# Optimization experiments

Hardware: AMD Instinct MI355X
Metric: run time of the kernel (lower is better)

## Reference

```python
import jax, jax.numpy as jnp
import numpy as np

N_NODES = 100000
N_EDGES = 600000
IN_F, HID_F, OUT_F = 128, 128, 64


def setup_inputs() -> dict:
    key = jax.random.key(0)
    ks = jax.random.split(key, 12)
    s = 0.05  # small init scale to keep activations bounded
    return {
        "features": jax.random.normal(ks[0], (N_NODES, IN_F), jnp.float32),
        "edge_src": jax.random.randint(ks[1], (N_EDGES,), 0, N_NODES, jnp.int32),
        "edge_dst": jax.random.randint(ks[2], (N_EDGES,), 0, N_NODES, jnp.int32),
        "W1": jax.random.normal(ks[3], (HID_F, 3 * IN_F), jnp.float32) * s,
        "b1": jnp.zeros((HID_F,), jnp.float32),
        "bn_gamma": jnp.ones((HID_F,), jnp.float32),
        "bn_beta": jnp.zeros((HID_F,), jnp.float32),
        "bn_mean": jnp.zeros((HID_F,), jnp.float32),
        "bn_var": jnp.ones((HID_F,), jnp.float32),
        "W3": jax.random.normal(ks[4], (HID_F, 3 * HID_F), jnp.float32) * s,
        "b3": jnp.zeros((HID_F,), jnp.float32),
        "Wm1": jax.random.normal(ks[5], (HID_F, HID_F), jnp.float32) * s,
        "bm1": jnp.zeros((HID_F,), jnp.float32),
        "Wm2": jax.random.normal(ks[6], (OUT_F, HID_F), jnp.float32) * s,
        "bm2": jnp.zeros((OUT_F,), jnp.float32),
    }


def _cheb_conv(x, W, b, src, dst, dinv, n):
    """DGL ChebConv with k=3, lambda_max=2 (re_norm=1).
    L f = f - D^-1/2 A D^-1/2 f  via gather-scatter on the edge list."""
    def lap(f):
        agg = jax.ops.segment_sum((f * dinv)[src], dst, num_segments=n)
        return f - agg * dinv
    X0 = x
    X1 = -lap(X0)                 # X1 = -re_norm*L(X0) + (re_norm-1)*X0, re_norm=1
    X2 = -2.0 * lap(X1) - X0      # X2 = -2*re_norm*L(X1) + 2*(re_norm-1)*X1 - X0
    Xt = jnp.concatenate([X0, X1, X2], axis=1)  # [n, 3*in]
    return Xt @ W.T + b


def reference(features, edge_src, edge_dst, W1, b1, bn_gamma, bn_beta,
              bn_mean, bn_var, W3, b3, Wm1, bm1, Wm2, bm2):
    n = features.shape[0]
    deg = jax.ops.segment_sum(jnp.ones_like(edge_dst, jnp.float32), edge_dst,
                              num_segments=n)
    dinv = jnp.clip(deg, 1.0, None) ** -0.5  # D^{-1/2}, in-degree (DGL)
    dinv = dinv[:, None]

    x = jax.nn.relu(_cheb_conv(features, W1, b1, edge_src, edge_dst, dinv, n))
    # BatchNorm1d (eval mode)
    x = (x - bn_mean) * jax.lax.rsqrt(bn_var + 1e-5) * bn_gamma + bn_beta
    # NOTE: original early-stopping loop never updates x -> dead code, omitted.
    x_res = x
    x = jax.nn.relu(_cheb_conv(x, W3, b3, edge_src, edge_dst, dinv, n))
    x = x + x_res  # dropout is identity in eval mode
    # MLP head
    h = jax.nn.relu(x @ Wm1.T + bm1)
    return h @ Wm2.T + bm2
```

## Files before the change

kernel.cpp:

```cpp
#include <hip/hip_runtime.h>
#include <cstdint>
#include <cstddef>

#define NF 128
#define SCAN_B 256

typedef __attribute__((ext_vector_type(4))) float f32x4;
typedef __attribute__((ext_vector_type(8))) short bf16x8;

#define GL2LDS16(g, l) __builtin_amdgcn_global_load_lds(                     \
    (const __attribute__((address_space(1))) unsigned*)(g),                  \
    (__attribute__((address_space(3))) unsigned*)(l), 16, 0, 0)

static __device__ inline float bf2f(short u) {
    union { unsigned u; float f; } v;
    v.u = ((unsigned)(unsigned short)u) << 16;
    return v.f;
}
static __device__ inline short f2bf(float f) {
    union { float f; unsigned u; } v; v.f = f;
    unsigned r = v.u + 0x7FFF + ((v.u >> 16) & 1);
    return (short)(r >> 16);
}
static __device__ inline float u2f(unsigned u) {
    union { unsigned u; float f; } v; v.u = u; return v.f;
}
static __device__ inline unsigned f2u(float f) {
    union { float f; unsigned u; } v; v.f = f; return v.u;
}
static __device__ inline unsigned packbf(float lo, float hi) {
    unsigned ul = f2u(lo), uh = f2u(hi);
    ul = ul + 0x7FFF + ((ul >> 16) & 1);
    uh = uh + 0x7FFF + ((uh >> 16) & 1);
    return (ul >> 16) | (uh & 0xFFFF0000u);
}


static __global__ __launch_bounds__(256) void k_pro(
    const int* __restrict__ dst, int ne, int* __restrict__ counts,
    const float* __restrict__ feat, short* __restrict__ fbf, int n8, int nbE, int nbF,
    const float* __restrict__ w1, const float* __restrict__ w3,
    const float* __restrict__ wm1, const float* __restrict__ wm2,
    short* __restrict__ o1, short* __restrict__ o3,
    short* __restrict__ om1, short* __restrict__ om2) {
    int b = blockIdx.x;
    if (b < nbE) {
        int e = b * 256 + threadIdx.x;
        if (e < ne) atomicAdd(&counts[dst[e]], 1);
        return;
    }
    b -= nbE;
    if (b < nbF) {
        int i = b * 256 + threadIdx.x;
        if (i < n8) {
            f32x4 a = *(const f32x4*)&feat[(size_t)i * 8];
            f32x4 c = *(const f32x4*)&feat[(size_t)i * 8 + 4];
            bf16x8 r;
            r[0] = f2bf(a[0]); r[1] = f2bf(a[1]); r[2] = f2bf(a[2]); r[3] = f2bf(a[3]);
            r[4] = f2bf(c[0]); r[5] = f2bf(c[1]); r[6] = f2bf(c[2]); r[7] = f2bf(c[3]);
            *(bf16x8*)&fbf[(size_t)i * 8] = r;
        }
        return;
    }
    b -= nbF;
    int i = b * 256 + threadIdx.x;
    if (i < 12288) {
        const float* x = (i < 6144) ? w1 : w3;
        short* y       = (i < 6144) ? o1 : o3;
        int ii = (i < 6144) ? i : i - 6144;
        int r = ii / 48, c = ii % 48;
        int kt = c * 8, seg = kt >> 7, o = kt & 127;
        const float* base = x + (size_t)r * 384;
        float c0, c1, c2;
        if (seg == 0)      { c0 = 1.f;  c1 = -1.f; c2 = 1.f;  }
        else if (seg == 1) { c0 = 0.f;  c1 = 1.f;  c2 = -4.f; }
        else               { c0 = 0.f;  c1 = 0.f;  c2 = 2.f;  }
        bf16x8 rr;
#pragma unroll
        for (int h = 0; h < 2; ++h) {
            f32x4 a0 = *(const f32x4*)&base[o + h * 4];
            f32x4 a1 = *(const f32x4*)&base[128 + o + h * 4];
            f32x4 a2 = *(const f32x4*)&base[256 + o + h * 4];
#pragma unroll
            for (int j = 0; j < 4; ++j)
                rr[h * 4 + j] = f2bf(c0 * a0[j] + c1 * a1[j] + c2 * a2[j]);
        }
        *(bf16x8*)&y[(size_t)r * 384 + kt] = rr;
        return;
    }
    const float* x; short* y; int off;
    if (i < 14336) { x = wm1; y = om1; off = i - 12288; }
    else           { x = wm2; y = om2; off = i - 14336; }
    f32x4 a = *(const f32x4*)&x[(size_t)off * 8];
    f32x4 c = *(const f32x4*)&x[(size_t)off * 8 + 4];
    bf16x8 r;
    r[0] = f2bf(a[0]); r[1] = f2bf(a[1]); r[2] = f2bf(a[2]); r[3] = f2bf(a[3]);
    r[4] = f2bf(c[0]); r[5] = f2bf(c[1]); r[6] = f2bf(c[2]); r[7] = f2bf(c[3]);
    *(bf16x8*)&y[(size_t)off * 8] = r;
}


static __global__ void k_scan1(const int* __restrict__ counts, int n,
                               int* __restrict__ row_off, int* __restrict__ bsum) {
    __shared__ int s[SCAN_B];
    int t = threadIdx.x;
    int base = blockIdx.x * SCAN_B;
    int v = (base + t < n) ? counts[base + t] : 0;
    s[t] = v;
    __syncthreads();
    for (int off = 1; off < SCAN_B; off <<= 1) {
        int x = 0;
        if (t >= off) x = s[t - off];
        __syncthreads();
        if (t >= off) s[t] += x;
        __syncthreads();
    }
    if (base + t < n) row_off[base + t] = s[t] - v;
    if (t == SCAN_B - 1) bsum[blockIdx.x] = s[t];
}

static __global__ void k_scan2(int* __restrict__ bsum, int nb) {
    __shared__ int s[512];
    int t = threadIdx.x;
    int v = (t < nb) ? bsum[t] : 0;
    s[t] = v;
    __syncthreads();
    for (int off = 1; off < 512; off <<= 1) {
        int x = 0;
        if (t >= off) x = s[t - off];
        __syncthreads();
        if (t >= off) s[t] += x;
        __syncthreads();
    }
    if (t < nb) bsum[t] = s[t] - v;
}

static __global__ void k_scan3(int* __restrict__ row_off, const int* __restrict__ bsum,
                               int n, int ne, int* __restrict__ cursor,
                               const int* __restrict__ counts, float* __restrict__ dinv) {
    int i = blockIdx.x * SCAN_B + threadIdx.x;
    if (i < n) {
        int v = row_off[i] + bsum[blockIdx.x];
        row_off[i] = v;
        cursor[i] = v;
        float d = fmaxf((float)counts[i], 1.0f);
        dinv[i] = rsqrtf(d);
    }
    if (i == 0) row_off[n] = ne;
}

static __global__ void k_fill(const int* __restrict__ src, const int* __restrict__ dst, int ne,
                              int* __restrict__ cursor, int2* __restrict__ csrw,
                              const float* __restrict__ dinv) {
    int e = blockIdx.x * blockDim.x + threadIdx.x;
    if (e < ne) {
        int d = dst[e];
        int s = src[e];
        int p = atomicAdd(&cursor[d], 1);
        csrw[p] = make_int2(s, (int)f2u(dinv[s]));
    }
}


static __global__ __launch_bounds__(256) void k_lap(
    const short* __restrict__ Xin,
    const int* __restrict__ row_off, const int2* __restrict__ csrw,
    const float* __restrict__ dinv,
    short* __restrict__ out, int n) {
    int node = blockIdx.x * 4 + (threadIdx.x >> 6);
    if (node >= n) return;
    int l = threadIdx.x & 63;
    const unsigned* Xu = (const unsigned*)Xin;
    int e0 = row_off[node], e1 = row_off[node + 1];
    int deg = e1 - e0;

    int myi = 0; int mydv = 0;
    if (l < deg && l < 64) {
        int2 q = csrw[e0 + l];
        myi = q.x; mydv = q.y;
    }

    float s0 = 0.f, s1 = 0.f;
    int dcap = deg < 64 ? deg : 64;
    for (int base = 0; base < dcap; base += 8) {
        unsigned v[8]; float dv[8];
#pragma unroll
        for (int j = 0; j < 8; ++j) {
            int jj = base + j;
            bool act = (jj < dcap);
            int lane = act ? jj : base;
            int src = __builtin_amdgcn_readlane(myi, lane);
            unsigned dvb = __builtin_amdgcn_readlane(mydv, lane);
            dv[j] = act ? u2f(dvb) : 0.f;
            v[j] = Xu[(size_t)src * 64 + l];
        }
#pragma unroll
        for (int j = 0; j < 8; ++j) {
            s0 += u2f(v[j] << 16) * dv[j];
            s1 += u2f(v[j] & 0xFFFF0000u) * dv[j];
        }
    }
    for (int base = e0 + 64; base < e1; base += 8) {
        int m = e1 - base;
        int2 qq = make_int2(0, 0);
        if (l < 8 && l < m) qq = csrw[base + l];
        unsigned v[8]; float dv[8];
#pragma unroll
        for (int j = 0; j < 8; ++j) {
            int src = __shfl(qq.x, j, 64);
            int dvb = __shfl(qq.y, j, 64);
            bool act = (j < m);
            if (!act) src = 0;
            dv[j] = act ? u2f((unsigned)dvb) : 0.f;
            v[j] = Xu[(size_t)src * 64 + l];
        }
#pragma unroll
        for (int j = 0; j < 8; ++j) {
            s0 += u2f(v[j] << 16) * dv[j];
            s1 += u2f(v[j] & 0xFFFF0000u) * dv[j];
        }
    }

    float di = dinv[node];
    ((unsigned*)out)[(size_t)node * 64 + l] = packbf(s0 * di, s1 * di);
}


static __global__ __launch_bounds__(512) void k_gemm_conv(
    const short* __restrict__ X0, const short* __restrict__ X1, const short* __restrict__ X2,
    const short* __restrict__ Wbf, const float* __restrict__ bias,
    const float* __restrict__ bng, const float* __restrict__ bnb,
    const float* __restrict__ bnm, const float* __restrict__ bnv,
    int M, short* __restrict__ out) {
    __shared__ short As[2][128 * 32];
    __shared__ short Bs[2][128 * 32];

    const int nwg = gridDim.x;
    const int q = nwg >> 3, r = nwg & 7;
    const int xcd = blockIdx.x & 7, slot = blockIdx.x >> 3;
    const int flat = (xcd < r ? xcd * (q + 1) : r * (q + 1) + (xcd - r) * q) + slot;
    const int m0 = flat * 128;

    const int t = threadIdx.x;
    const int wv = t >> 6;
    const int ln = t & 63;
    const int wr = wv >> 2;
    const int wc = wv & 3;
    const int lr = ln & 15;
    const int lk = ln >> 4;

    const short* segs[3] = {X0, X1, X2};

    f32x4 acc[4][2];
#pragma unroll
    for (int i = 0; i < 4; ++i)
#pragma unroll
        for (int j = 0; j < 2; ++j) acc[i][j] = (f32x4){0.f, 0.f, 0.f, 0.f};

    auto issue = [&](int buf, int kt) {
        const short* Xp = segs[kt >> 7];
        const int klocal = kt & 127;
#pragma unroll
        for (int j = 0; j < 2; ++j) {
            int g = wv * 2 + j;
            int c = g * 64 + ln;
            if (g < 8) {
                int row = c >> 2, sl = c & 3;
                int gm = m0 + row;
                if (gm > M - 1) gm = M - 1;
                const short* src = &Xp[(size_t)gm * 128 + klocal + ((sl ^ ((row >> 1) & 3)) * 8)];
                GL2LDS16(src, &As[buf][g * 512]);
            } else {
                int cb = c - 512;
                int row = cb >> 2, sl = cb & 3;
                const short* src = &Wbf[(size_t)row * 384 + kt + ((sl ^ ((row >> 1) & 3)) * 8)];
                GL2LDS16(src, &Bs[buf][(g - 8) * 512]);
            }
        }
    };
    auto compute = [&](int buf) {
        bf16x8 af[4], bfr[2];
#pragma unroll
        for (int fi = 0; fi < 4; ++fi) {
            int row = wr * 64 + fi * 16 + lr;
            af[fi] = *(const bf16x8*)&As[buf][row * 32 + ((lk ^ ((row >> 1) & 3)) * 8)];
        }
#pragma unroll
        for (int fj = 0; fj < 2; ++fj) {
            int row = wc * 32 + fj * 16 + lr;
            bfr[fj] = *(const bf16x8*)&Bs[buf][row * 32 + ((lk ^ ((row >> 1) & 3)) * 8)];
        }
#pragma unroll
        for (int fi = 0; fi < 4; ++fi)
#pragma unroll
            for (int fj = 0; fj < 2; ++fj)
                acc[fi][fj] = __builtin_amdgcn_mfma_f32_16x16x32_bf16(af[fi], bfr[fj], acc[fi][fj], 0, 0, 0);
    };

    issue(0, 0);
    __syncthreads();
#pragma unroll
    for (int tgt = 0; tgt < 12; ++tgt) {
        if (tgt < 11) issue((tgt + 1) & 1, (tgt + 1) * 32);
        compute(tgt & 1);
        __syncthreads();
    }

#pragma unroll
    for (int fi = 0; fi < 4; ++fi) {
#pragma unroll
        for (int reg = 0; reg < 4; ++reg) {
            int gm = m0 + wr * 64 + fi * 16 + lk * 4 + reg;
            if (gm >= M) continue;
#pragma unroll
            for (int fj = 0; fj < 2; ++fj) {
                int gn = wc * 32 + fj * 16 + lr;
                float y = fmaxf(acc[fi][fj][reg] + bias[gn], 0.f);
                float sc = rsqrtf(bnv[gn] + 1e-5f) * bng[gn];
                y = (y - bnm[gn]) * sc + bnb[gn];
                out[(size_t)gm * 128 + gn] = f2bf(y);
            }
        }
    }
}


static __global__ __launch_bounds__(512) void k_gemm_mlp(
    const short* __restrict__ X0, const short* __restrict__ X1, const short* __restrict__ X2,
    const short* __restrict__ Wbf, const float* __restrict__ bias,
    const short* __restrict__ res,
    const short* __restrict__ Wm1bf, const float* __restrict__ bm1,
    const short* __restrict__ Wm2bf, const float* __restrict__ bm2,
    int M, float* __restrict__ out) {
    __shared__ __align__(16) short smem[25600];
    short* As0 = smem;
    short* As1 = smem + 4096;
    short* Bs0 = smem + 8192;
    short* Bs1 = smem + 12288;
    short* hs  = smem;
    short* Wst = smem + 17408;

    const int nwg = gridDim.x;
    const int q = nwg >> 3, r = nwg & 7;
    const int xcd = blockIdx.x & 7, slot = blockIdx.x >> 3;
    const int flat = (xcd < r ? xcd * (q + 1) : r * (q + 1) + (xcd - r) * q) + slot;
    const int m0 = flat * 128;

    const int t = threadIdx.x;
    const int wv = t >> 6;
    const int ln = t & 63;
    const int wr = wv >> 2;
    const int wc = wv & 3;
    const int lr = ln & 15;
    const int lk = ln >> 4;

    const short* segs[3] = {X0, X1, X2};

    f32x4 acc[4][2];
#pragma unroll
    for (int i = 0; i < 4; ++i)
#pragma unroll
        for (int j = 0; j < 2; ++j) acc[i][j] = (f32x4){0.f, 0.f, 0.f, 0.f};

    auto issue = [&](int buf, int kt) {
        const short* Xp = segs[kt >> 7];
        const int klocal = kt & 127;
        short* Ab = buf ? As1 : As0;
        short* Bb = buf ? Bs1 : Bs0;
#pragma unroll
        for (int j = 0; j < 2; ++j) {
            int g = wv * 2 + j;
            int c = g * 64 + ln;
            if (g < 8) {
                int row = c >> 2, sl = c & 3;
                int gm = m0 + row;
                if (gm > M - 1) gm = M - 1;
                const short* src = &Xp[(size_t)gm * 128 + klocal + ((sl ^ ((row >> 1) & 3)) * 8)];
                GL2LDS16(src, &Ab[g * 512]);
            } else {
                int cb = c - 512;
                int row = cb >> 2, sl = cb & 3;
                const short* src = &Wbf[(size_t)row * 384 + kt + ((sl ^ ((row >> 1) & 3)) * 8)];
                GL2LDS16(src, &Bb[(g - 8) * 512]);
            }
        }
    };
    auto compute = [&](int buf) {
        short* Ab = buf ? As1 : As0;
        short* Bb = buf ? Bs1 : Bs0;
        bf16x8 af[4], bfr[2];
#pragma unroll
        for (int fi = 0; fi < 4; ++fi) {
            int row = wr * 64 + fi * 16 + lr;
            af[fi] = *(const bf16x8*)&Ab[row * 32 + ((lk ^ ((row >> 1) & 3)) * 8)];
        }
#pragma unroll
        for (int fj = 0; fj < 2; ++fj) {
            int row = wc * 32 + fj * 16 + lr;
            bfr[fj] = *(const bf16x8*)&Bb[row * 32 + ((lk ^ ((row >> 1) & 3)) * 8)];
        }
#pragma unroll
        for (int fi = 0; fi < 4; ++fi)
#pragma unroll
            for (int fj = 0; fj < 2; ++fj)
                acc[fi][fj] = __builtin_amdgcn_mfma_f32_16x16x32_bf16(af[fi], bfr[fj], acc[fi][fj], 0, 0, 0);
    };

    issue(0, 0);
    __syncthreads();
#pragma unroll
    for (int tgt = 0; tgt < 12; ++tgt) {
        if (tgt < 11) issue((tgt + 1) & 1, (tgt + 1) * 32);
        compute(tgt & 1);
        __syncthreads();
    }

    auto issueW1 = [&](int buf, int kt) {
        int c = t;
        int row = c >> 2, sl = c & 3;
        const short* src = &Wm1bf[(size_t)row * 128 + kt + ((sl ^ ((row >> 1) & 3)) * 8)];
        GL2LDS16(src, &Wst[buf * 4096 + c * 8]);
    };
    issueW1(0, 0);

#pragma unroll
    for (int fi = 0; fi < 4; ++fi) {
#pragma unroll
        for (int reg = 0; reg < 4; ++reg) {
            int row = wr * 64 + fi * 16 + lk * 4 + reg;
            int gm = m0 + row;
            int gr = gm < M ? gm : M - 1;
#pragma unroll
            for (int fj = 0; fj < 2; ++fj) {
                int gn = wc * 32 + fj * 16 + lr;
                float y = fmaxf(acc[fi][fj][reg] + bias[gn], 0.f) + bf2f(res[(size_t)gr * 128 + gn]);
                hs[row * 136 + gn] = f2bf(y);
            }
        }
    }
    __syncthreads();

    f32x4 acc2[4][2];
#pragma unroll
    for (int i = 0; i < 4; ++i)
#pragma unroll
        for (int j = 0; j < 2; ++j) acc2[i][j] = (f32x4){0.f, 0.f, 0.f, 0.f};

#pragma unroll
    for (int s = 0; s < 4; ++s) {
        if (s < 3) issueW1((s + 1) & 1, (s + 1) * 32);
        int kt = s * 32;
        short* Wb = &Wst[(s & 1) * 4096];
        bf16x8 af[4], bw[2];
#pragma unroll
        for (int fi = 0; fi < 4; ++fi) {
            int row = wr * 64 + fi * 16 + lr;
            af[fi] = *(const bf16x8*)&hs[row * 136 + kt + lk * 8];
        }
#pragma unroll
        for (int fj = 0; fj < 2; ++fj) {
            int row = wc * 32 + fj * 16 + lr;
            bw[fj] = *(const bf16x8*)&Wb[row * 32 + ((lk ^ ((row >> 1) & 3)) * 8)];
        }
#pragma unroll
        for (int fi = 0; fi < 4; ++fi)
#pragma unroll
            for (int fj = 0; fj < 2; ++fj)
                acc2[fi][fj] = __builtin_amdgcn_mfma_f32_16x16x32_bf16(af[fi], bw[fj], acc2[fi][fj], 0, 0, 0);
        __syncthreads();
    }

#pragma unroll
    for (int j = 0; j < 2; ++j) {
        int c = j * 512 + t;
        int row = c >> 4, s = c & 15;
        const short* src = &Wm2bf[(size_t)row * 128 + ((s ^ (row & 7)) * 8)];
        GL2LDS16(src, &Wst[c * 8]);
    }
#pragma unroll
    for (int fi = 0; fi < 4; ++fi) {
#pragma unroll
        for (int reg = 0; reg < 4; ++reg) {
            int row = wr * 64 + fi * 16 + lk * 4 + reg;
#pragma unroll
            for (int fj = 0; fj < 2; ++fj) {
                int col = wc * 32 + fj * 16 + lr;
                hs[row * 136 + col] = f2bf(fmaxf(acc2[fi][fj][reg] + bm1[col], 0.f));
            }
        }
    }
    __syncthreads();

    f32x4 acc3[4];
#pragma unroll
    for (int i = 0; i < 4; ++i) acc3[i] = (f32x4){0.f, 0.f, 0.f, 0.f};
#pragma unroll
    for (int s = 0; s < 4; ++s) {
        int kt = s * 32;
        bf16x8 af, bw;
        int brow = wc * 16 + lr;
        int sidx = s * 4 + lk;
        bw = *(const bf16x8*)&Wst[brow * 128 + ((sidx ^ (brow & 7)) * 8)];
#pragma unroll
        for (int fi = 0; fi < 4; ++fi) {
            int row = wr * 64 + fi * 16 + lr;
            af = *(const bf16x8*)&hs[row * 136 + kt + lk * 8];
            acc3[fi] = __builtin_amdgcn_mfma_f32_16x16x32_bf16(af, bw, acc3[fi], 0, 0, 0);
        }
    }

#pragma unroll
    for (int fi = 0; fi < 4; ++fi) {
#pragma unroll
        for (int reg = 0; reg < 4; ++reg) {
            int gm = m0 + wr * 64 + fi * 16 + lk * 4 + reg;
            if (gm >= M) continue;
            int col = wc * 16 + lr;
            out[(size_t)gm * 64 + col] = acc3[fi][reg] + bm2[col];
        }
    }
}


extern "C" void kernel_launch(void* const* d_in, const int* in_sizes, int n_in,
                              void* d_out, int out_size, void* d_ws, size_t ws_size,
                              hipStream_t stream) {
    const float* features = (const float*)d_in[0];
    const int*   esrc     = (const int*)d_in[1];
    const int*   edst     = (const int*)d_in[2];
    const float* W1   = (const float*)d_in[3];
    const float* b1   = (const float*)d_in[4];
    const float* bng  = (const float*)d_in[5];
    const float* bnb  = (const float*)d_in[6];
    const float* bnm  = (const float*)d_in[7];
    const float* bnv  = (const float*)d_in[8];
    const float* W3   = (const float*)d_in[9];
    const float* b3   = (const float*)d_in[10];
    const float* Wm1  = (const float*)d_in[11];
    const float* bm1  = (const float*)d_in[12];
    const float* Wm2  = (const float*)d_in[13];
    const float* bm2  = (const float*)d_in[14];
    float* out = (float*)d_out;

    const int n  = in_sizes[0] / NF;
    const int ne = in_sizes[1];

    uint8_t* w = (uint8_t*)d_ws;
    size_t off = 0;
    auto alloc = [&](size_t bytes) -> void* {
        void* p = w + off;
        off = (off + bytes + 255) & ~(size_t)255;
        return p;
    };
    float* dinv   = (float*)alloc((size_t)n * 4);
    int* counts   = (int*)alloc((size_t)n * 4);
    int* row_off  = (int*)alloc(((size_t)n + 1) * 4);
    int* cursor   = (int*)alloc((size_t)n * 4);
    int2* csrw    = (int2*)alloc((size_t)ne * 8);
    int* bsum     = (int*)alloc(4096);
    short* fbf    = (short*)alloc((size_t)n * NF * 2);
    short* bufB   = (short*)alloc((size_t)n * NF * 2);
    short* bufC   = (short*)alloc((size_t)n * NF * 2);
    short* bufD   = (short*)alloc((size_t)n * NF * 2);
    short* W1bf   = (short*)alloc((size_t)128 * 384 * 2);
    short* W3bf   = (short*)alloc((size_t)128 * 384 * 2);
    short* Wm1bf  = (short*)alloc((size_t)128 * 128 * 2);
    short* Wm2bf  = (short*)alloc((size_t)64 * 128 * 2);
    (void)ws_size;

    const int TB = 256;
    const int nbE = (ne + TB - 1) / TB;
    const int nbN = (n + TB - 1) / TB;
    const int n8  = n * NF / 8;
    const int nbF = (n8 + TB - 1) / TB;

    hipMemsetAsync(counts, 0, (size_t)n * 4, stream);
    k_pro<<<nbE + nbF + 60, TB, 0, stream>>>(edst, ne, counts,
                                             features, fbf, n8, nbE, nbF,
                                             W1, W3, Wm1, Wm2, W1bf, W3bf, Wm1bf, Wm2bf);
    k_scan1<<<nbN, SCAN_B, 0, stream>>>(counts, n, row_off, bsum);
    k_scan2<<<1, 512, 0, stream>>>(bsum, nbN);
    k_scan3<<<nbN, SCAN_B, 0, stream>>>(row_off, bsum, n, ne, cursor, counts, dinv);
    k_fill<<<nbE, TB, 0, stream>>>(esrc, edst, ne, cursor, csrw, dinv);

    const int gm128 = (n + 127) / 128;
    const int nbL   = (n + 3) / 4;

    k_lap<<<nbL, 256, 0, stream>>>(fbf, row_off, csrw, dinv, bufB, n);
    k_lap<<<nbL, 256, 0, stream>>>(bufB, row_off, csrw, dinv, bufC, n);
    k_gemm_conv<<<gm128, 512, 0, stream>>>(fbf, bufB, bufC, W1bf, b1,
                                           bng, bnb, bnm, bnv, n, bufD);

    k_lap<<<nbL, 256, 0, stream>>>(bufD, row_off, csrw, dinv, bufB, n);
    k_lap<<<nbL, 256, 0, stream>>>(bufB, row_off, csrw, dinv, bufC, n);
    k_gemm_mlp<<<gm128, 512, 0, stream>>>(bufD, bufB, bufC, W3bf, b3, bufD,
                                          Wm1bf, bm1, Wm2bf, bm2, n, out);
}
```

Before: 283.2 us.

## Replace CSR build with fixed-width ELL adjacency plus overflow list

```diff
diff --git a/kernel.cpp b/kernel.cpp
--- a/kernel.cpp
+++ b/kernel.cpp
@@ -3,7 +3,7 @@
 #include <cstddef>
 
 #define NF 128
-#define SCAN_B 256
+#define OVF_CAP 65536
 
 typedef __attribute__((ext_vector_type(4))) float f32x4;
 typedef __attribute__((ext_vector_type(8))) short bf16x8;
@@ -25,6 +25,7 @@
 static __device__ inline float u2f(unsigned u) {
     union { unsigned u; float f; } v; v.u = u; return v.f;
 }
+static __device__ inline float f2u_f(unsigned u) { return u2f(u); }
 static __device__ inline unsigned f2u(float f) {
     union { float f; unsigned u; } v; v.f = f; return v.u;
 }
@@ -37,7 +38,9 @@
 
 
 static __global__ __launch_bounds__(256) void k_pro(
-    const int* __restrict__ dst, int ne, int* __restrict__ counts,
+    const int* __restrict__ esrc, const int* __restrict__ edst, int ne,
+    int* __restrict__ cnt, int* __restrict__ ell,
+    int* __restrict__ ovf_cnt, int2* __restrict__ ovf,
     const float* __restrict__ feat, short* __restrict__ fbf, int n8, int nbE, int nbF,
     const float* __restrict__ w1, const float* __restrict__ w3,
     const float* __restrict__ wm1, const float* __restrict__ wm2,
@@ -46,7 +49,15 @@
     int b = blockIdx.x;
     if (b < nbE) {
         int e = b * 256 + threadIdx.x;
-        if (e < ne) atomicAdd(&counts[dst[e]], 1);
+        if (e < ne) {
+            int d = edst[e], s = esrc[e];
+            int r = atomicAdd(&cnt[d], 1);
+            if (r < 64) ell[(size_t)d * 64 + r] = s;
+            else {
+                int o = atomicAdd(ovf_cnt, 1);
+                if (o < OVF_CAP) ovf[o] = make_int2(d, s);
+            }
+        }
         return;
     }
     b -= nbE;
@@ -100,88 +111,25 @@
 }
 
 
-static __global__ void k_scan1(const int* __restrict__ counts, int n,
-                               int* __restrict__ row_off, int* __restrict__ bsum) {
-    __shared__ int s[SCAN_B];
-    int t = threadIdx.x;
-    int base = blockIdx.x * SCAN_B;
-    int v = (base + t < n) ? counts[base + t] : 0;
-    s[t] = v;
-    __syncthreads();
-    for (int off = 1; off < SCAN_B; off <<= 1) {
-        int x = 0;
-        if (t >= off) x = s[t - off];
-        __syncthreads();
-        if (t >= off) s[t] += x;
-        __syncthreads();
-    }
-    if (base + t < n) row_off[base + t] = s[t] - v;
-    if (t == SCAN_B - 1) bsum[blockIdx.x] = s[t];
-}
-
-static __global__ void k_scan2(int* __restrict__ bsum, int nb) {
-    __shared__ int s[512];
-    int t = threadIdx.x;
-    int v = (t < nb) ? bsum[t] : 0;
-    s[t] = v;
-    __syncthreads();
-    for (int off = 1; off < 512; off <<= 1) {
-        int x = 0;
-        if (t >= off) x = s[t - off];
-        __syncthreads();
-        if (t >= off) s[t] += x;
-        __syncthreads();
-    }
-    if (t < nb) bsum[t] = s[t] - v;
-}
-
-static __global__ void k_scan3(int* __restrict__ row_off, const int* __restrict__ bsum,
-                               int n, int ne, int* __restrict__ cursor,
-                               const int* __restrict__ counts, float* __restrict__ dinv) {
-    int i = blockIdx.x * SCAN_B + threadIdx.x;
-    if (i < n) {
-        int v = row_off[i] + bsum[blockIdx.x];
-        row_off[i] = v;
-        cursor[i] = v;
-        float d = fmaxf((float)counts[i], 1.0f);
-        dinv[i] = rsqrtf(d);
-    }
-    if (i == 0) row_off[n] = ne;
-}
-
-static __global__ void k_fill(const int* __restrict__ src, const int* __restrict__ dst, int ne,
-                              int* __restrict__ cursor, int2* __restrict__ csrw,
-                              const float* __restrict__ dinv) {
-    int e = blockIdx.x * blockDim.x + threadIdx.x;
-    if (e < ne) {
-        int d = dst[e];
-        int s = src[e];
-        int p = atomicAdd(&cursor[d], 1);
-        csrw[p] = make_int2(s, (int)f2u(dinv[s]));
-    }
-}
-
-
 static __global__ __launch_bounds__(256) void k_lap(
     const short* __restrict__ Xin,
-    const int* __restrict__ row_off, const int2* __restrict__ csrw,
-    const float* __restrict__ dinv,
+    const int* __restrict__ cnt, const int* __restrict__ ell,
+    const int* __restrict__ ovf_cnt, const int2* __restrict__ ovf,
     short* __restrict__ out, int n) {
     int node = blockIdx.x * 4 + (threadIdx.x >> 6);
     if (node >= n) return;
     int l = threadIdx.x & 63;
     const unsigned* Xu = (const unsigned*)Xin;
-    int e0 = row_off[node], e1 = row_off[node + 1];
-    int deg = e1 - e0;
-
-    int myi = 0; int mydv = 0;
-    if (l < deg && l < 64) {
-        int2 q = csrw[e0 + l];
-        myi = q.x; mydv = q.y;
+    int deg = cnt[node];
+    int dcap = deg < 64 ? deg : 64;
+
+    int myi = 0; float mydv = 0.f;
+    if (l < dcap) {
+        myi = ell[(size_t)node * 64 + l];
+        mydv = rsqrtf(fmaxf((float)cnt[myi], 1.f));
     }
 
     float s0 = 0.f, s1 = 0.f;
-    int dcap = deg < 64 ? deg : 64;
     for (int base = 0; base < dcap; base += 8) {
         unsigned v[8]; float dv[8];
 #pragma unroll
@@ -190,7 +138,7 @@
             bool act = (jj < dcap);
             int lane = act ? jj : base;
             int src = __builtin_amdgcn_readlane(myi, lane);
-            unsigned dvb = __builtin_amdgcn_readlane(mydv, lane);
+            unsigned dvb = __builtin_amdgcn_readlane((int)f2u(mydv), lane);
             dv[j] = act ? u2f(dvb) : 0.f;
             v[j] = Xu[(size_t)src * 64 + l];
         }
@@ -200,28 +148,21 @@
             s1 += u2f(v[j] & 0xFFFF0000u) * dv[j];
         }
     }
-    for (int base = e0 + 64; base < e1; base += 8) {
-        int m = e1 - base;
-        int2 qq = make_int2(0, 0);
-        if (l < 8 && l < m) qq = csrw[base + l];
-        unsigned v[8]; float dv[8];
-#pragma unroll
-        for (int j = 0; j < 8; ++j) {
-            int src = __shfl(qq.x, j, 64);
-            int dvb = __shfl(qq.y, j, 64);
-            bool act = (j < m);
-            if (!act) src = 0;
-            dv[j] = act ? u2f((unsigned)dvb) : 0.f;
-            v[j] = Xu[(size_t)src * 64 + l];
-        }
-#pragma unroll
-        for (int j = 0; j < 8; ++j) {
-            s0 += u2f(v[j] << 16) * dv[j];
-            s1 += u2f(v[j] & 0xFFFF0000u) * dv[j];
-        }
-    }
-
-    float di = dinv[node];
+    int novf = *ovf_cnt;
+    if (novf > 0) {
+        if (novf > OVF_CAP) novf = OVF_CAP;
+        for (int k = 0; k < novf; ++k) {
+            int2 q2 = ovf[k];
+            if (q2.x == node) {
+                float dw = rsqrtf(fmaxf((float)cnt[q2.y], 1.f));
+                unsigned v = Xu[(size_t)q2.y * 64 + l];
+                s0 += u2f(v << 16) * dw;
+                s1 += u2f(v & 0xFFFF0000u) * dw;
+            }
+        }
+    }
+
+    float di = rsqrtf(fmaxf((float)deg, 1.f));
     ((unsigned*)out)[(size_t)node * 64 + l] = packbf(s0 * di, s1 * di);
 }
 
@@ -552,12 +493,9 @@
         off = (off + bytes + 255) & ~(size_t)255;
         return p;
     };
-    float* dinv   = (float*)alloc((size_t)n * 4);
-    int* counts   = (int*)alloc((size_t)n * 4);
-    int* row_off  = (int*)alloc(((size_t)n + 1) * 4);
-    int* cursor   = (int*)alloc((size_t)n * 4);
-    int2* csrw    = (int2*)alloc((size_t)ne * 8);
-    int* bsum     = (int*)alloc(4096);
+    int* cnt      = (int*)alloc(((size_t)n + 1) * 4);
+    int* ell      = (int*)alloc((size_t)n * 64 * 4);
+    int2* ovf     = (int2*)alloc((size_t)OVF_CAP * 8);
     short* fbf    = (short*)alloc((size_t)n * NF * 2);
     short* bufB   = (short*)alloc((size_t)n * NF * 2);
     short* bufC   = (short*)alloc((size_t)n * NF * 2);
@@ -567,32 +505,28 @@
     short* Wm1bf  = (short*)alloc((size_t)128 * 128 * 2);
     short* Wm2bf  = (short*)alloc((size_t)64 * 128 * 2);
     (void)ws_size;
+    int* ovf_cnt = cnt + n;
 
     const int TB = 256;
     const int nbE = (ne + TB - 1) / TB;
-    const int nbN = (n + TB - 1) / TB;
     const int n8  = n * NF / 8;
     const int nbF = (n8 + TB - 1) / TB;
 
-    hipMemsetAsync(counts, 0, (size_t)n * 4, stream);
-    k_pro<<<nbE + nbF + 60, TB, 0, stream>>>(edst, ne, counts,
+    hipMemsetAsync(cnt, 0, ((size_t)n + 1) * 4, stream);
+    k_pro<<<nbE + nbF + 60, TB, 0, stream>>>(esrc, edst, ne, cnt, ell, ovf_cnt, ovf,
                                              features, fbf, n8, nbE, nbF,
                                              W1, W3, Wm1, Wm2, W1bf, W3bf, Wm1bf, Wm2bf);
-    k_scan1<<<nbN, SCAN_B, 0, stream>>>(counts, n, row_off, bsum);
-    k_scan2<<<1, 512, 0, stream>>>(bsum, nbN);
-    k_scan3<<<nbN, SCAN_B, 0, stream>>>(row_off, bsum, n, ne, cursor, counts, dinv);
-    k_fill<<<nbE, TB, 0, stream>>>(esrc, edst, ne, cursor, csrw, dinv);
 
     const int gm128 = (n + 127) / 128;
     const int nbL   = (n + 3) / 4;
 
-    k_lap<<<nbL, 256, 0, stream>>>(fbf, row_off, csrw, dinv, bufB, n);
-    k_lap<<<nbL, 256, 0, stream>>>(bufB, row_off, csrw, dinv, bufC, n);
+    k_lap<<<nbL, 256, 0, stream>>>(fbf, cnt, ell, ovf_cnt, ovf, bufB, n);
+    k_lap<<<nbL, 256, 0, stream>>>(bufB, cnt, ell, ovf_cnt, ovf, bufC, n);
     k_gemm_conv<<<gm128, 512, 0, stream>>>(fbf, bufB, bufC, W1bf, b1,
                                            bng, bnb, bnm, bnv, n, bufD);
 
-    k_lap<<<nbL, 256, 0, stream>>>(bufD, row_off, csrw, dinv, bufB, n);
-    k_lap<<<nbL, 256, 0, stream>>>(bufB, row_off, csrw, dinv, bufC, n);
+    k_lap<<<nbL, 256, 0, stream>>>(bufD, cnt, ell, ovf_cnt, ovf, bufB, n);
+    k_lap<<<nbL, 256, 0, stream>>>(bufB, cnt, ell, ovf_cnt, ovf, bufC, n);
     k_gemm_mlp<<<gm128, 512, 0, stream>>>(bufD, bufB, bufC, W3bf, b3, bufD,
                                           Wm1bf, bm1, Wm2bf, bm2, n, out);
 }
```

Measured after the change: 261.9 us. 1.08x faster.
